# Performance work log

Measured on AMD Instinct MI355X. Metric: run time of the kernel, lower is better.

The kernel has to match this reference:

```python
import jax, jax.numpy as jnp
import numpy as np

B, T, D = 8, 1024, 16
QUANTILE = 0.5
EPS_T = 1e-6


def setup_inputs() -> dict:
    key = jax.random.key(0)
    k1, k2 = jax.random.split(key)
    z = jax.random.normal(k1, (B, T, D), dtype=jnp.float32)
    variances = jax.random.uniform(k2, (B, T, D), dtype=jnp.float32)
    length_scales = jnp.ones((D,), dtype=jnp.float32)  # nn.Parameter init
    sigmas = jnp.ones((D,), dtype=jnp.float32)         # nn.Parameter init
    return {"z": z, "variances": variances,
            "length_scales": length_scales, "sigmas": sigmas}


def reference(z, variances, length_scales, sigmas):
    b, t, d = z.shape
    dt = z.dtype
    N = b * t
    zf = z.reshape(N, d)          # [N, D] flattened per-dim samples
    vf = variances.reshape(N, d)  # [N, D]

    # quantile-threshold mask per latent dim (linear-interp quantile, as torch)
    thr = jnp.quantile(vf, QUANTILE, axis=0)          # [D]
    m = (vf <= thr).astype(dt)                        # [N, D] 0/1 mask

    # time index for every flattened point: arange(T) tiled over batch
    tt = jnp.tile(jnp.arange(t, dtype=dt), b)         # [N]
    # pairwise weight W_ij = 1 / (|t_i - t_j| + eps); shared across dims
    W = 1.0 / (jnp.abs(tt[:, None] - tt[None, :]) + EPS_T)  # [N, N]

    # masked pairwise mean of (z_i - z_j)^2 * W_ij, algebraically:
    #   sum_ij m_i m_j (z_i - z_j)^2 W_ij = 2 (u^T W m - v^T W v)
    # with u = m*z^2, v = m*z (diagonal contributes 0 since m^2 = m).
    V = m * zf                                        # [N, D]
    U = V * zf                                        # [N, D]
    WM = W @ jnp.concatenate([m, V], axis=1)          # [N, 2D] single GEMM
    Wm, WV = WM[:, :d], WM[:, d:]
    S = 2.0 * (jnp.sum(U * Wm, axis=0) - jnp.sum(V * WV, axis=0))  # [D]

    n = jnp.sum(m, axis=0)                            # [D] selected counts
    mean_ratio = S / (n * n)                          # mean over N_sel^2 pairs
    ls_est = jax.lax.stop_gradient(jnp.sqrt(mean_ratio))  # .detach() in torch

    # (unbiased variance estimate; only used for 'cauchy' kernel, kept for parity)
    mu = jnp.sum(V, axis=0) / n
    var_est = jax.lax.stop_gradient(
        jnp.sum(m * (zf - mu[None, :]) ** 2, axis=0) / (n - 1.0))

    enough = n >= 2.0
    length_scale = jnp.where(enough, ls_est, jnp.exp(length_scales))  # [D]
    _sigma = jnp.where(enough, var_est, jnp.exp(sigmas))  # unused for rbf

    # rbf kernel per dim: exp(-(ti - tj)^2 / ls^2), [D, T, T]
    ts = jnp.arange(t, dtype=dt)
    dist2 = (ts[None, :] - ts[:, None]) ** 2          # [T, T]
    K = jnp.exp(-dist2[None, :, :] / (length_scale[:, None, None] ** 2))
    # repeat over batch -> [B, D, T, T] (covariance of the MVN prior; loc is 0)
    return jnp.broadcast_to(K[None], (b, d, t, t))
```

## Files before the change

kernel.cpp:

```cpp
#include <hip/hip_runtime.h>

typedef float vfloat4 __attribute__((ext_vector_type(4)));

#define TT 1024
#define BB 8
#define DD 16
#define NN 8192

__device__ inline float untr(unsigned u) {
    unsigned b = (u & 0x80000000u) ? (u & 0x7fffffffu) : ~u;
    return __uint_as_float(b);
}

__global__ __launch_bounds__(1024) void median_k(const float* __restrict__ v,
                                                 float* __restrict__ thr,
                                                 float* __restrict__ Sacc,
                                                 float* __restrict__ nacc) {
    __shared__ unsigned key[NN];
    __shared__ unsigned hist[2048];
    __shared__ unsigned wsum[16];
    __shared__ unsigned found_bin, found_cum;
    __shared__ unsigned s_cle, s_min;
    const int d = blockIdx.x;
    const int tid = threadIdx.x;
    const int wid = tid >> 6, lane = tid & 63;

    if (tid == 0) { Sacc[d] = 0.f; nacc[d] = 0.f; }

    for (int i = tid; i < NN; i += 1024) {
        unsigned b = __float_as_uint(v[i * DD + d]);
        key[i] = (b & 0x80000000u) ? ~b : (b | 0x80000000u);
    }
    if (tid == 0) { s_cle = 0; s_min = 0xFFFFFFFFu; }
    __syncthreads();

    unsigned prefix = 0;
    unsigned r = 4095;
    int matched_bits = 0;
    int shift = 32;
    const int chunk_bits[3] = {11, 11, 10};
#pragma unroll
    for (int pass = 0; pass < 3; ++pass) {
        const int bits = chunk_bits[pass];
        shift -= bits;
        const int nb = 1 << bits;
        hist[tid] = 0; hist[tid + 1024] = 0;
        __syncthreads();
        for (int i = tid; i < NN; i += 1024) {
            unsigned k = key[i];
            if (matched_bits == 0 || (k >> (shift + bits)) == prefix)
                atomicAdd(&hist[(k >> shift) & (unsigned)(nb - 1)], 1u);
        }
        __syncthreads();
        unsigned h0 = 0, h1 = 0, s2 = 0;
        if (tid < nb / 2) { h0 = hist[2 * tid]; h1 = hist[2 * tid + 1]; s2 = h0 + h1; }
        unsigned inc = s2;
        for (int o = 1; o < 64; o <<= 1) {
            unsigned t = __shfl_up(inc, o);
            if (lane >= o) inc += t;
        }
        if (lane == 63) wsum[wid] = inc;
        __syncthreads();
        if (tid < 16) {
            unsigned x = wsum[tid], ix = x;
            for (int o = 1; o < 16; o <<= 1) {
                unsigned t = __shfl_up(ix, o);
                if (lane >= o) ix += t;
            }
            wsum[tid] = ix - x;
        }
        __syncthreads();
        if (tid < nb / 2) {
            unsigned cum = wsum[wid] + (inc - s2);
            if (r >= cum && r < cum + h0)            { found_bin = 2u * tid;     found_cum = cum; }
            else if (r >= cum + h0 && r < cum + s2)  { found_bin = 2u * tid + 1; found_cum = cum + h0; }
        }
        __syncthreads();
        prefix = (prefix << bits) | found_bin;
        r -= found_cum;
        matched_bits += bits;
    }
    const unsigned A = prefix;

    unsigned cle = 0, mg = 0xFFFFFFFFu;
    for (int i = tid; i < NN; i += 1024) {
        unsigned k = key[i];
        if (k <= A) cle++;
        else mg = min(mg, k);
    }
    for (int o = 32; o; o >>= 1) {
        cle += __shfl_xor(cle, o);
        mg = min(mg, (unsigned)__shfl_xor(mg, o));
    }
    if (lane == 0) { atomicAdd(&s_cle, cle); atomicMin(&s_min, mg); }
    __syncthreads();
    if (tid == 0) {
        unsigned Bk = (s_cle >= 4097u) ? A : s_min;
        thr[d] = 0.5f * (untr(A) + untr(Bk));
    }
}

__global__ __launch_bounds__(64) void stats_k(const float* __restrict__ z,
                                              const float* __restrict__ v,
                                              const float* __restrict__ thr,
                                              float* __restrict__ Sacc,
                                              float* __restrict__ nacc) {
    __shared__ float sm[TT], sv[TT], wt[TT];
    const int d = blockIdx.x >> 4;
    const int chunk = blockIdx.x & 15;
    const int tid = threadIdx.x;
    const int p = chunk * 64 + tid;
    const float t = thr[d];

    float su = 0.f;
    for (int q = tid; q < TT; q += 64) {
        float s_m = 0.f, s_v = 0.f, s_u = 0.f;
#pragma unroll
        for (int b = 0; b < BB; ++b) {
            const float vv = v[b * (TT * DD) + q * DD + d];
            const float zz = z[b * (TT * DD) + q * DD + d];
            if (vv <= t) { s_m += 1.f; s_v += zz; s_u += zz * zz; }
        }
        sm[q] = s_m; sv[q] = s_v;
        wt[q] = 1.0f / ((float)q + 1e-6f);
        if (q == p) su = s_u;
    }
    __syncthreads();

    const float a = su;
    const float c = sv[p];
    float acc = 0.f;
#pragma unroll 4
    for (int q = 0; q < TT; ++q) {
        int ad = p - q; ad = ad < 0 ? -ad : ad;
        acc = fmaf(wt[ad], fmaf(a, sm[q], -(c * sv[q])), acc);
    }
    float npart = sm[p];
    for (int o = 32; o; o >>= 1) {
        acc += __shfl_xor(acc, o);
        npart += __shfl_xor(npart, o);
    }
    if (tid == 0) {
        atomicAdd(&Sacc[d], 2.0f * acc);
        atomicAdd(&nacc[d], npart);
    }
}

__global__ __launch_bounds__(256) void write_k(const float* __restrict__ Sacc,
                                               const float* __restrict__ nacc,
                                               const float* __restrict__ lsin,
                                               float* __restrict__ out) {
    const int bid = blockIdx.x;
    const int d = bid >> 10;
    const int i = bid & (TT - 1);

    const float n = nacc[d], S = Sacc[d];
    float inv;
    if (n >= 2.0f) inv = (n * n) / S;
    else { const float e = __expf(lsin[d]); inv = 1.0f / (e * e); }

    const int j0 = threadIdx.x * 4;
    vfloat4 val;
#pragma unroll
    for (int jj = 0; jj < 4; ++jj) {
        const int diff = (j0 + jj) - i;
        const float f = (float)(diff * diff);
        val[jj] = __expf(-f * inv);
    }
    const size_t base = ((size_t)d << 20) | ((size_t)i << 10) | (size_t)j0;
#pragma unroll
    for (int b = 0; b < BB; ++b) {
        vfloat4* p = (vfloat4*)(out + ((size_t)b << 24) + base);
        __builtin_nontemporal_store(val, p);
    }
}

extern "C" void kernel_launch(void* const* d_in, const int* in_sizes, int n_in,
                              void* d_out, int out_size, void* d_ws, size_t ws_size,
                              hipStream_t stream) {
    const float* z    = (const float*)d_in[0];
    const float* v    = (const float*)d_in[1];
    const float* lsin = (const float*)d_in[2];
    float* out = (float*)d_out;

    float* ws   = (float*)d_ws;
    float* thr  = ws;
    float* Sacc = ws + 16;
    float* nacc = ws + 32;

    median_k<<<DD, 1024, 0, stream>>>(v, thr, Sacc, nacc);
    stats_k<<<DD * 16, 64, 0, stream>>>(z, v, thr, Sacc, nacc);
    write_k<<<DD * TT, 256, 0, stream>>>(Sacc, nacc, lsin, out);
}
```

Before: 632.3 us.

## Fuse per-time masked reductions into median kernel and pack shared arrays

The masked per-time sums (count, z sum, z^2 sum) move into the median kernel, which already holds the variance keys in shared memory. They are written to workspace, so the second kernel no longer re-reads z and v 16 times per dimension. The pairwise loop now reads the mask count and z sum as one float2 from shared memory. In exchange the median kernel, which runs on only 16 blocks, does a little more serial work.

```diff
diff --git a/kernel.cpp b/kernel.cpp
--- a/kernel.cpp
+++ b/kernel.cpp
@@ -11,26 +11,32 @@
     unsigned b = (u & 0x80000000u) ? (u & 0x7fffffffu) : ~u;
     return __uint_as_float(b);
 }
+__device__ inline unsigned tr(float f) {
+    unsigned b = __float_as_uint(f);
+    return (b & 0x80000000u) ? ~b : (b | 0x80000000u);
+}
 
 __global__ __launch_bounds__(1024) void median_k(const float* __restrict__ v,
+                                                 const float* __restrict__ z,
                                                  float* __restrict__ thr,
                                                  float* __restrict__ Sacc,
-                                                 float* __restrict__ nacc) {
+                                                 float* __restrict__ nacc,
+                                                 float* __restrict__ ms_t,
+                                                 float* __restrict__ vs_t,
+                                                 float* __restrict__ us_t) {
     __shared__ unsigned key[NN];
     __shared__ unsigned hist[2048];
     __shared__ unsigned wsum[16];
     __shared__ unsigned found_bin, found_cum;
-    __shared__ unsigned s_cle, s_min;
+    __shared__ unsigned s_cle, s_min, s_keythr;
     const int d = blockIdx.x;
     const int tid = threadIdx.x;
     const int wid = tid >> 6, lane = tid & 63;
 
     if (tid == 0) { Sacc[d] = 0.f; nacc[d] = 0.f; }
 
-    for (int i = tid; i < NN; i += 1024) {
-        unsigned b = __float_as_uint(v[i * DD + d]);
-        key[i] = (b & 0x80000000u) ? ~b : (b | 0x80000000u);
-    }
+    for (int i = tid; i < NN; i += 1024)
+        key[i] = tr(v[i * DD + d]);
     if (tid == 0) { s_cle = 0; s_min = 0xFFFFFFFFu; }
     __syncthreads();
 
@@ -96,46 +102,51 @@
     __syncthreads();
     if (tid == 0) {
         unsigned Bk = (s_cle >= 4097u) ? A : s_min;
-        thr[d] = 0.5f * (untr(A) + untr(Bk));
-    }
-}
-
-__global__ __launch_bounds__(64) void stats_k(const float* __restrict__ z,
-                                              const float* __restrict__ v,
-                                              const float* __restrict__ thr,
+        const float th = 0.5f * (untr(A) + untr(Bk));
+        thr[d] = th;
+        s_keythr = tr(th);
+    }
+    __syncthreads();
+
+    const unsigned kt = s_keythr;
+    float s_m = 0.f, s_v = 0.f, s_u = 0.f;
+#pragma unroll
+    for (int b = 0; b < BB; ++b) {
+        const unsigned k = key[b * TT + tid];
+        const float zz = z[(b * TT + tid) * DD + d];
+        if (k <= kt) { s_m += 1.f; s_v += zz; s_u += zz * zz; }
+    }
+    ms_t[d * TT + tid] = s_m;
+    vs_t[d * TT + tid] = s_v;
+    us_t[d * TT + tid] = s_u;
+}
+
+__global__ __launch_bounds__(64) void scale_k(const float* __restrict__ ms_t,
+                                              const float* __restrict__ vs_t,
+                                              const float* __restrict__ us_t,
                                               float* __restrict__ Sacc,
                                               float* __restrict__ nacc) {
-    __shared__ float sm[TT], sv[TT], wt[TT];
+    __shared__ float2 smsv[TT];
+    __shared__ float wt[TT];
     const int d = blockIdx.x >> 4;
     const int chunk = blockIdx.x & 15;
     const int tid = threadIdx.x;
+    for (int q = tid; q < TT; q += 64) {
+        smsv[q] = make_float2(ms_t[d * TT + q], vs_t[d * TT + q]);
+        wt[q] = 1.0f / ((float)q + 1e-6f);
+    }
+    __syncthreads();
     const int p = chunk * 64 + tid;
-    const float t = thr[d];
-
-    float su = 0.f;
-    for (int q = tid; q < TT; q += 64) {
-        float s_m = 0.f, s_v = 0.f, s_u = 0.f;
-#pragma unroll
-        for (int b = 0; b < BB; ++b) {
-            const float vv = v[b * (TT * DD) + q * DD + d];
-            const float zz = z[b * (TT * DD) + q * DD + d];
-            if (vv <= t) { s_m += 1.f; s_v += zz; s_u += zz * zz; }
-        }
-        sm[q] = s_m; sv[q] = s_v;
-        wt[q] = 1.0f / ((float)q + 1e-6f);
-        if (q == p) su = s_u;
-    }
-    __syncthreads();
-
-    const float a = su;
-    const float c = sv[p];
+    const float a = us_t[d * TT + p];
+    const float c = smsv[p].y;
     float acc = 0.f;
 #pragma unroll 4
     for (int q = 0; q < TT; ++q) {
         int ad = p - q; ad = ad < 0 ? -ad : ad;
-        acc = fmaf(wt[ad], fmaf(a, sm[q], -(c * sv[q])), acc);
-    }
-    float npart = sm[p];
+        const float2 x = smsv[q];
+        acc = fmaf(wt[ad], fmaf(a, x.x, -(c * x.y)), acc);
+    }
+    float npart = smsv[p].x;
     for (int o = 32; o; o >>= 1) {
         acc += __shfl_xor(acc, o);
         npart += __shfl_xor(npart, o);
@@ -187,8 +198,11 @@
     float* thr  = ws;
     float* Sacc = ws + 16;
     float* nacc = ws + 32;
-
-    median_k<<<DD, 1024, 0, stream>>>(v, thr, Sacc, nacc);
-    stats_k<<<DD * 16, 64, 0, stream>>>(z, v, thr, Sacc, nacc);
+    float* ms_t = ws + 64;
+    float* vs_t = ms_t + TT * DD;
+    float* us_t = vs_t + TT * DD;
+
+    median_k<<<DD, 1024, 0, stream>>>(v, z, thr, Sacc, nacc, ms_t, vs_t, us_t);
+    scale_k<<<DD * 16, 64, 0, stream>>>(ms_t, vs_t, us_t, Sacc, nacc);
     write_k<<<DD * TT, 256, 0, stream>>>(Sacc, nacc, lsin, out);
 }
```

Result: faster. 572.1 us (-9.5%).
